# Kernel tuning notes

Hardware: AMD Instinct MI355X
Metric: run time of the kernel (lower is better)

The kernel has to match this reference:

```python
import jax, jax.numpy as jnp
import numpy as np
import math

SAMPLE_RATIO = 0.25
K = 5
EPS = 1e-6

def _cells(loc_orig, H, W):
    # map normalized [-1,1] coords to nearest grid cell index, as in tcformer token2map/map2token
    loc = jnp.clip(loc_orig, -1.0, 1.0)
    px = jnp.clip(jnp.round(0.5 * (loc[..., 0] + 1.0) * W - 0.5).astype(jnp.int32), 0, W - 1)
    py = jnp.clip(jnp.round(0.5 * (loc[..., 1] + 1.0) * H - 0.5).astype(jnp.int32), 0, H - 1)
    return py * W + px  # [B, N0]

def token2map(x, loc_orig, idx_agg, H, W):
    B, N, C = x.shape
    N0 = loc_orig.shape[1]
    cell = _cells(loc_orig, H, W)
    seg = (cell + jnp.arange(B)[:, None] * (H * W)).reshape(-1)
    feat = x[jnp.arange(B)[:, None], idx_agg]  # [B, N0, C] token feature per original point
    sums = jax.ops.segment_sum(feat.reshape(-1, C), seg, num_segments=B * H * W)
    cnt = jax.ops.segment_sum(jnp.ones((B * N0,), x.dtype), seg, num_segments=B * H * W)
    x_map = sums / (cnt[:, None] + EPS)  # per-cell mean over points hitting the cell
    return x_map.reshape(B, H, W, C).transpose(0, 3, 1, 2)

def map2token(x_map, N, loc_orig, idx_agg, agg_weight):
    B, C, H, W = x_map.shape
    cell = _cells(loc_orig, H, W)
    val = x_map.reshape(B, C, H * W).transpose(0, 2, 1)  # [B, HW, C]
    vpt = val[jnp.arange(B)[:, None], cell]              # [B, N0, C] map value at each point
    seg = (idx_agg + jnp.arange(B)[:, None] * N).reshape(-1)
    w = agg_weight.reshape(-1)
    wsum = jax.ops.segment_sum(w, seg, num_segments=B * N) + EPS
    ssum = jax.ops.segment_sum(vpt.reshape(-1, C) * w[:, None], seg, num_segments=B * N)
    return (ssum / wsum[:, None]).reshape(B, N, C)  # agg_weight-weighted mean per token

def token_cluster_merge(x, Ns, idx_agg, weight, k):
    B, N, C = x.shape
    # DPC-KNN clustering (index computation; mirrors torch.no_grad block)
    sq = jnp.sum(x * x, -1)
    d2 = jnp.clip(sq[:, :, None] + sq[:, None, :] - 2.0 * jnp.einsum('bnc,bmc->bnm', x, x), 0.0, None)
    dist = jnp.sqrt(d2) / (C ** 0.5)
    dnear = -jax.lax.top_k(-dist, k)[0]                  # k smallest distances (incl. self)
    density = jnp.exp(-jnp.mean(dnear * dnear, -1))
    mask = density[:, None, :] > density[:, :, None]
    dmax = jnp.max(dist.reshape(B, -1), -1)[:, None, None]
    parent_dist = jnp.min(jnp.where(mask, dist, dmax), -1)  # dist to nearest higher-density token
    score = parent_dist * density
    index_down = jax.lax.top_k(score, Ns)[1]             # [B, Ns] cluster centers
    idx_cluster = jnp.argmin(dist[jnp.arange(B)[:, None], index_down], axis=1)  # [B, N]
    idx_cluster = idx_cluster.at[jnp.arange(B)[:, None], index_down].set(jnp.arange(Ns)[None, :])
    # weighted merge of tokens into clusters
    seg = (idx_cluster + jnp.arange(B)[:, None] * Ns).reshape(-1)
    w = weight.reshape(-1)
    allw = jax.ops.segment_sum(w, seg, num_segments=B * Ns) + EPS
    norm_w = (w / allw[seg]).reshape(B, N)
    x_merged = jax.ops.segment_sum((x * norm_w[:, :, None]).reshape(-1, C), seg, num_segments=B * Ns).reshape(B, Ns, C)
    idx_agg_down = idx_cluster[jnp.arange(B)[:, None], idx_agg]      # compose index maps
    weight_t = norm_w[jnp.arange(B)[:, None], idx_agg][..., None]    # [B, N0, 1]
    return x_merged, idx_agg_down, weight_t

def _forward(x, loc_orig, idx_agg, agg_weight, idx_k_loc, H, W, conv_w, conv_b, skip_w, ln_g, ln_b, conf_w, conf_b):
    B, N, C = x.shape
    x_map = token2map(x, loc_orig, idx_agg, H, W)
    x_map = jax.lax.conv_general_dilated(x_map, conv_w, (2, 2), ((1, 1), (1, 1))) + conv_b[None, :, None, None]
    x_tok = map2token(x_map, N, loc_orig, idx_agg, agg_weight) + jnp.einsum('bnc,oc->bno', x, skip_w)
    mu = jnp.mean(x_tok, -1, keepdims=True)
    var = jnp.mean((x_tok - mu) ** 2, -1, keepdims=True)
    x_tok = (x_tok - mu) / jnp.sqrt(var + 1e-5) * ln_g + ln_b
    conf = jnp.einsum('bnc,oc->bno', x_tok, conf_w) + conf_b
    weight = jnp.exp(conf)
    Ns = max(math.ceil(N * SAMPLE_RATIO), 1)
    x_down, idx_agg_down, weight_t = token_cluster_merge(x_tok, Ns, idx_agg, weight, K)
    agg_weight_down = agg_weight * weight_t
    agg_weight_down = agg_weight_down / jnp.max(agg_weight_down, axis=1, keepdims=True)
    # down_block is an injected submodule; treated as identity passthrough here
    return x_down, idx_agg_down, agg_weight_down

def setup_inputs():
    key = jax.random.key(0)
    ks = jax.random.split(key, 8)
    B, N, C, N0, Cout = 8, 256, 256, 16384, 512
    return {
        'x': jax.random.normal(ks[0], (B, N, C), jnp.float32),
        'loc_orig': jax.random.uniform(ks[1], (B, N0, 2), jnp.float32, -1.0, 1.0),
        'idx_agg': jax.random.randint(ks[2], (B, N0), 0, N),
        'agg_weight': jax.random.uniform(ks[3], (B, N0, 1), jnp.float32, 0.1, 1.0),
        'idx_k_loc': jax.random.randint(ks[4], (B, N0, K), 0, N0),
        'H': 64, 'W': 64,
        'conv_w': jax.random.normal(ks[5], (Cout, C, 3, 3), jnp.float32) * 0.02,
        'conv_b': jnp.zeros((Cout,), jnp.float32),
        'skip_w': jax.random.normal(ks[6], (Cout, C), jnp.float32) * 0.02,
        'ln_g': jnp.ones((Cout,), jnp.float32),
        'ln_b': jnp.zeros((Cout,), jnp.float32),
        'conf_w': jax.random.normal(ks[7], (1, Cout), jnp.float32) * 0.02,
        'conf_b': jnp.zeros((1,), jnp.float32),
    }

def reference(x, loc_orig, idx_agg, agg_weight, idx_k_loc, H, W, conv_w, conv_b, skip_w, ln_g, ln_b, conf_w, conf_b):
    return _forward(x, loc_orig, idx_agg, agg_weight, idx_k_loc, H, W, conv_w, conv_b, skip_w, ln_g, ln_b, conf_w, conf_b)
```

## Files before the change

### kernel.cpp

```cpp
#include <hip/hip_runtime.h>
#include <math.h>

typedef unsigned long long ull;
typedef __attribute__((ext_vector_type(8))) short short8v;
typedef __attribute__((ext_vector_type(4))) float float4v;

#define NB   8
#define NTOK 256
#define CIN  256
#define NP   16384
#define NCO  512
#define HW64 4096
#define OHW  1024
#define NS   64
#define EPS  1e-6f
#define KC   2304

constexpr size_t OFF_SUMS = 0;
constexpr size_t OFF_CNT  = OFF_SUMS + (size_t)NB*HW64*CIN;
constexpr size_t OFF_AMAT = OFF_CNT  + (size_t)NB*HW64;
constexpr size_t OFF_ALLW = OFF_AMAT + (size_t)NB*NTOK*OHW;
constexpr size_t OFF_DMAX = OFF_ALLW + (size_t)NB*NS;
constexpr size_t OFF_MAXW = OFF_DMAX + NB;
constexpr size_t ZERO_END = OFF_MAXW + NB;
constexpr size_t OFF_WT   = ZERO_END;
constexpr size_t OFF_SKWT = OFF_WT   + (size_t)KC*NCO;
constexpr size_t OFF_Y    = OFF_SKWT + (size_t)CIN*NCO;
constexpr size_t OFF_C2   = OFF_Y    + (size_t)NB*OHW*NCO;
constexpr size_t OFF_WSUM = OFF_C2   + (size_t)NB*NTOK*NCO;
constexpr size_t OFF_XSKIP= OFF_WSUM + (size_t)NB*NTOK;
constexpr size_t OFF_XTOK = OFF_XSKIP+ (size_t)NB*NTOK*NCO;
constexpr size_t OFF_XPK  = OFF_XTOK + (size_t)NB*NTOK*NCO;
constexpr size_t OFF_WEXP = OFF_XPK  + (size_t)NB*NTOK*NCO;
constexpr size_t OFF_SQ   = OFF_WEXP + (size_t)NB*NTOK;
constexpr size_t OFF_DIST = OFF_SQ   + (size_t)NB*NTOK;
constexpr size_t OFF_DENS = OFF_DIST + (size_t)NB*NTOK*NTOK;
constexpr size_t OFF_SCORE= OFF_DENS + (size_t)NB*NTOK;
constexpr size_t OFF_IND  = OFF_SCORE+ (size_t)NB*NTOK;
constexpr size_t OFF_IDXCL= OFF_IND  + (size_t)NB*NS;
constexpr size_t OFF_NORMW= OFF_IDXCL+ (size_t)NB*NTOK;
constexpr size_t OFF_AWBUF= OFF_NORMW+ (size_t)NB*NTOK;
constexpr size_t OFF_XTPK = OFF_AWBUF+ (size_t)NB*NP;
constexpr size_t OFF_AMATP = OFF_SUMS;
constexpr size_t OFF_XTOKPK= OFF_Y;

__device__ __forceinline__ unsigned pack_hl(float x) {
    unsigned u = __float_as_uint(x);
    unsigned t = u + 0x7fffu + ((u >> 16) & 1u);
    unsigned hibits = t & 0xffff0000u;
    float lo = x - __uint_as_float(hibits);
    unsigned ul = __float_as_uint(lo);
    unsigned lt = ul + 0x7fffu + ((ul >> 16) & 1u);
    return hibits | (lt >> 16);
}
__device__ __forceinline__ unsigned hp2(unsigned w0, unsigned w1) {
    return __builtin_amdgcn_perm(w1, w0, 0x07060302u);
}
__device__ __forceinline__ unsigned lp2(unsigned w0, unsigned w1) {
    return __builtin_amdgcn_perm(w1, w0, 0x05040100u);
}

__global__ void hist(const float* __restrict__ loc, const int* __restrict__ idxagg,
                     const float* __restrict__ aggw,
                     int* __restrict__ cntmat, float* __restrict__ cnt,
                     float* __restrict__ amat) {
    int bp = blockIdx.x*256 + threadIdx.x;
    int b  = bp >> 14;
    float lx = loc[2*bp+0], ly = loc[2*bp+1];
    lx = fminf(fmaxf(lx, -1.f), 1.f);
    ly = fminf(fmaxf(ly, -1.f), 1.f);
    int px = (int)rintf((lx + 1.f)*32.f - 0.5f); px = min(max(px,0),63);
    int py = (int)rintf((ly + 1.f)*32.f - 0.5f); py = min(max(py,0),63);
    int cell = py*64 + px;
    int tok = idxagg[bp];
    atomicAdd(&cntmat[((size_t)(b*HW64 + cell))*NTOK + tok], 1);
    atomicAdd(&cnt[b*HW64 + cell], 1.0f);
    int qx = (int)rintf((lx + 1.f)*16.f - 0.5f); qx = min(max(qx,0),31);
    int qy = (int)rintf((ly + 1.f)*16.f - 0.5f); qy = min(max(qy,0),31);
    atomicAdd(&amat[((size_t)(b*NTOK + tok))*OHW + qy*32 + qx], aggw[bp]);
}

__global__ void cnt_pack(unsigned* __restrict__ m) {
    size_t i = (size_t)blockIdx.x*256 + threadIdx.x;
    int4 v = ((const int4*)m)[i];
    uint4 o;
    o.x = pack_hl((float)v.x); o.y = pack_hl((float)v.y);
    o.z = pack_hl((float)v.z); o.w = pack_hl((float)v.w);
    ((uint4*)m)[i] = o;
}

__global__ void xt_pack(const float* __restrict__ x, unsigned* __restrict__ xtpk) {
    int id = blockIdx.x*256 + threadIdx.x;
    int tok = id & 255, cin = (id >> 8) & 255, b = id >> 16;
    xtpk[id] = pack_hl(x[((size_t)(b*NTOK + tok))*CIN + cin]);
}

__global__ void wtrans(const float* __restrict__ convw, unsigned* __restrict__ wt) {
    int id = blockIdx.x*256 + threadIdx.x;
    int cout = id / KC, k = id - cout*KC;
    int grp = k >> 8, cin = k & 255;
    wt[id] = pack_hl(convw[(size_t)cout*KC + cin*9 + grp]);
}

__global__ void pack4(const float4* __restrict__ src, uint4* __restrict__ dst) {
    size_t i = (size_t)blockIdx.x*256 + threadIdx.x;
    float4 v = src[i];
    uint4 o;
    o.x = pack_hl(v.x); o.y = pack_hl(v.y); o.z = pack_hl(v.z); o.w = pack_hl(v.w);
    dst[i] = o;
}

__launch_bounds__(256)
__global__ void conv_gemm(const unsigned* __restrict__ xmap, const unsigned* __restrict__ wt,
                          const float* __restrict__ convb, unsigned* __restrict__ ytp) {
    __shared__ __align__(16) unsigned short Ahi[4096], Alo[4096];
    __shared__ __align__(16) unsigned short Bhi[2048], Blo[2048];
    int n0 = blockIdx.x * 128;
    int m0 = blockIdx.y * 64;
    int t = threadIdx.x;
    int lane = t & 63, wid = t >> 6;
    int wm = wid >> 1, wn = wid & 1;
    int l15 = lane & 15, l4 = lane >> 4;

    int rowL = t & 127, kg = t >> 7;
    int posG = n0 + rowL;
    int bb = posG >> 10, rem = posG & 1023;
    int oy = rem >> 5, ox = rem & 31;
    int rowB = t & 63, kgB = t >> 6;
    const unsigned* brow = wt + (size_t)(m0 + rowB)*KC + kgB*8;

    int wbA0 = (rowL>>4)*512 + kg*128 + (rowL&15)*8;
    int wbA1 = wbA0 + 256;
    int wbB  = (rowB>>4)*512 + kgB*128 + (rowB&15)*8;

    float4v acc[4][2] = {};
    uint4 a00,a01,a10,a11, b0,b1;

    auto loadA = [&](int kc) {
        int grp = kc >> 3;
        int ky = grp/3, kx = grp - 3*ky;
        int iy = 2*oy - 1 + ky, ix = 2*ox - 1 + kx;
        if ((unsigned)iy < 64u && (unsigned)ix < 64u) {
            const unsigned* ap = xmap + ((((size_t)bb*64 + iy)*64 + ix)*256 + (kc&7)*32 + kg*8);
            a00 = *(const uint4*)ap;       a01 = *(const uint4*)(ap + 4);
            a10 = *(const uint4*)(ap + 16); a11 = *(const uint4*)(ap + 20);
        } else {
            a00 = make_uint4(0,0,0,0); a01 = a00; a10 = a00; a11 = a00;
        }
    };
    auto loadB = [&](int kc) {
        const unsigned* bp = brow + (size_t)kc*32;
        b0 = *(const uint4*)bp; b1 = *(const uint4*)(bp + 4);
    };
    loadA(0); loadB(0);

    for (int kc = 0; kc < KC/32; ++kc) {
        __syncthreads();
        uint4 h, l;
        h.x=hp2(a00.x,a00.y); h.y=hp2(a00.z,a00.w); h.z=hp2(a01.x,a01.y); h.w=hp2(a01.z,a01.w);
        l.x=lp2(a00.x,a00.y); l.y=lp2(a00.z,a00.w); l.z=lp2(a01.x,a01.y); l.w=lp2(a01.z,a01.w);
        *(uint4*)&Ahi[wbA0] = h; *(uint4*)&Alo[wbA0] = l;
        h.x=hp2(a10.x,a10.y); h.y=hp2(a10.z,a10.w); h.z=hp2(a11.x,a11.y); h.w=hp2(a11.z,a11.w);
        l.x=lp2(a10.x,a10.y); l.y=lp2(a10.z,a10.w); l.z=lp2(a11.x,a11.y); l.w=lp2(a11.z,a11.w);
        *(uint4*)&Ahi[wbA1] = h; *(uint4*)&Alo[wbA1] = l;
        h.x=hp2(b0.x,b0.y); h.y=hp2(b0.z,b0.w); h.z=hp2(b1.x,b1.y); h.w=hp2(b1.z,b1.w);
        l.x=lp2(b0.x,b0.y); l.y=lp2(b0.z,b0.w); l.z=lp2(b1.x,b1.y); l.w=lp2(b1.z,b1.w);
        *(uint4*)&Bhi[wbB] = h; *(uint4*)&Blo[wbB] = l;
        __syncthreads();
        if (kc + 1 < KC/32) { loadA(kc+1); loadB(kc+1); }

        short8v bh[2], bl[2];
        #pragma unroll
        for (int q = 0; q < 2; ++q) {
            int off = (wn*2 + q)*512 + l4*128 + l15*8;
            bh[q] = *(const short8v*)&Bhi[off];
            bl[q] = *(const short8v*)&Blo[off];
        }
        #pragma unroll
        for (int p = 0; p < 4; ++p) {
            int off = (wm*4 + p)*512 + l4*128 + l15*8;
            short8v ah = *(const short8v*)&Ahi[off];
            short8v al = *(const short8v*)&Alo[off];
            #pragma unroll
            for (int q = 0; q < 2; ++q) {
                acc[p][q] = __builtin_amdgcn_mfma_f32_16x16x32_bf16(ah, bh[q], acc[p][q], 0, 0, 0);
                acc[p][q] = __builtin_amdgcn_mfma_f32_16x16x32_bf16(ah, bl[q], acc[p][q], 0, 0, 0);
                acc[p][q] = __builtin_amdgcn_mfma_f32_16x16x32_bf16(al, bh[q], acc[p][q], 0, 0, 0);
            }
        }
    }

    int bbk = n0 >> 10;
    int pos0 = (n0 & 1023) + wm*64;
    #pragma unroll
    for (int p = 0; p < 4; ++p) {
        int posb = pos0 + p*16 + l4*4;
        #pragma unroll
        for (int q = 0; q < 2; ++q) {
            int col = m0 + wn*32 + q*16 + l15;
            float bv = convb[col];
            uint4 o;
            o.x = pack_hl(acc[p][q][0] + bv);
            o.y = pack_hl(acc[p][q][1] + bv);
            o.z = pack_hl(acc[p][q][2] + bv);
            o.w = pack_hl(acc[p][q][3] + bv);
            *(uint4*)&ytp[((size_t)(bbk*NCO + col))*OHW + posb] = o;
        }
    }
}

template<int MODE, int TM, int TN>
__launch_bounds__(256)
__global__ void gemm_pk(const unsigned* __restrict__ A, const unsigned* __restrict__ B,
                        float* __restrict__ C, int K, int N,
                        long sA, long sB, long sC,
                        const float* __restrict__ aux, unsigned* __restrict__ dmaxU) {
    constexpr int NA = TM/64, NBs = TN/64;
    constexpr int WSM = TM/64;
    constexpr int WSN = 4/WSM;
    constexpr int TWM = TM/WSM, TWN = TN/WSN;
    constexpr int P = TWM/16, Q = TWN/16;
    __shared__ __align__(16) unsigned short Ahi[TM*32], Alo[TM*32];
    __shared__ __align__(16) unsigned short Bhi[TN*32], Blo[TN*32];
    int z = blockIdx.z;
    const unsigned* Ab = A + (size_t)z*sA;
    const unsigned* Bb = B + (size_t)z*sB;
    float* Cb = C + (size_t)z*sC;
    int n0 = blockIdx.x*TN, m0 = blockIdx.y*TM;
    int t = threadIdx.x;
    int lane = t & 63, wid = t >> 6;
    int wm = (WSM==2) ? (wid >> 1) : 0;
    int wn = (WSM==2) ? (wid & 1)  : wid;
    int l15 = lane & 15, l4 = lane >> 4;

    int rowA = t & (TM-1), kgA = t / TM;
    int rowB = t & (TN-1), kgB = t / TN;
    const unsigned* arow = Ab + (size_t)(m0 + rowA)*K + kgA*8;
    const unsigned* brw  = Bb + (size_t)(n0 + rowB)*K + kgB*8;
    int wbA = (rowA>>4)*512 + kgA*128 + (rowA&15)*8;
    int wbB = (rowB>>4)*512 + kgB*128 + (rowB&15)*8;

    float4v acc[P][Q] = {};
    uint4 ra[NA][2], rb[NBs][2];
    auto loadA = [&](int kc) {
        #pragma unroll
        for (int s = 0; s < NA; ++s) {
            const unsigned* p = arow + (size_t)kc*32 + s*16;
            ra[s][0] = *(const uint4*)p; ra[s][1] = *(const uint4*)(p + 4);
        }
    };
    auto loadB = [&](int kc) {
        #pragma unroll
        for (int s = 0; s < NBs; ++s) {
            const unsigned* p = brw + (size_t)kc*32 + s*16;
            rb[s][0] = *(const uint4*)p; rb[s][1] = *(const uint4*)(p + 4);
        }
    };
    loadA(0); loadB(0);
    int nkc = K >> 5;

    for (int kc = 0; kc < nkc; ++kc) {
        __syncthreads();
        uint4 h, l;
        #pragma unroll
        for (int s = 0; s < NA; ++s) {
            uint4 u0 = ra[s][0], u1 = ra[s][1];
            h.x=hp2(u0.x,u0.y); h.y=hp2(u0.z,u0.w); h.z=hp2(u1.x,u1.y); h.w=hp2(u1.z,u1.w);
            l.x=lp2(u0.x,u0.y); l.y=lp2(u0.z,u0.w); l.z=lp2(u1.x,u1.y); l.w=lp2(u1.z,u1.w);
            *(uint4*)&Ahi[wbA + s*256] = h; *(uint4*)&Alo[wbA + s*256] = l;
        }
        #pragma unroll
        for (int s = 0; s < NBs; ++s) {
            uint4 u0 = rb[s][0], u1 = rb[s][1];
            h.x=hp2(u0.x,u0.y); h.y=hp2(u0.z,u0.w); h.z=hp2(u1.x,u1.y); h.w=hp2(u1.z,u1.w);
            l.x=lp2(u0.x,u0.y); l.y=lp2(u0.z,u0.w); l.z=lp2(u1.x,u1.y); l.w=lp2(u1.z,u1.w);
            *(uint4*)&Bhi[wbB + s*256] = h; *(uint4*)&Blo[wbB + s*256] = l;
        }
        __syncthreads();
        if (kc + 1 < nkc) { loadA(kc+1); loadB(kc+1); }

        short8v bh[Q], bl[Q];
        #pragma unroll
        for (int q = 0; q < Q; ++q) {
            int off = (wn*Q + q)*512 + l4*128 + l15*8;
            bh[q] = *(const short8v*)&Bhi[off];
            bl[q] = *(const short8v*)&Blo[off];
        }
        #pragma unroll
        for (int p = 0; p < P; ++p) {
            int off = (wm*P + p)*512 + l4*128 + l15*8;
            short8v ah = *(const short8v*)&Ahi[off];
            short8v al = *(const short8v*)&Alo[off];
            #pragma unroll
            for (int q = 0; q < Q; ++q) {
                acc[p][q] = __builtin_amdgcn_mfma_f32_16x16x32_bf16(ah, bh[q], acc[p][q], 0, 0, 0);
                acc[p][q] = __builtin_amdgcn_mfma_f32_16x16x32_bf16(ah, bl[q], acc[p][q], 0, 0, 0);
                acc[p][q] = __builtin_amdgcn_mfma_f32_16x16x32_bf16(al, bh[q], acc[p][q], 0, 0, 0);
            }
        }
    }

    if (MODE == 0) {
        #pragma unroll
        for (int p = 0; p < P; ++p) {
            int mb = m0 + wm*TWM + p*16 + l4*4;
            #pragma unroll
            for (int q = 0; q < Q; ++q) {
                int n = n0 + wn*TWN + q*16 + l15;
                #pragma unroll
                for (int r = 0; r < 4; ++r)
                    Cb[(size_t)(mb + r)*N + n] = acc[p][q][r];
            }
        }
    } else if (MODE == 1) {
        const float inv = 1.0f / sqrtf(512.0f);
        const float* sqb = aux + (size_t)z*NTOK;
        float tmax = 0.f;
        #pragma unroll
        for (int p = 0; p < P; ++p) {
            int mb = m0 + wm*TWM + p*16 + l4*4;
            #pragma unroll
            for (int q = 0; q < Q; ++q) {
                int n = n0 + wn*TWN + q*16 + l15;
                float sn = sqb[n];
                #pragma unroll
                for (int r = 0; r < 4; ++r) {
                    float d2 = sqb[mb + r] + sn - 2.0f*acc[p][q][r];
                    float d = sqrtf(fmaxf(d2, 0.0f)) * inv;
                    Cb[(size_t)(mb + r)*N + n] = d;
                    tmax = fmaxf(tmax, d);
                }
            }
        }
        __shared__ float redm[4];
        #pragma unroll
        for (int off = 32; off; off >>= 1) tmax = fmaxf(tmax, __shfl_xor(tmax, off, 64));
        if (lane == 0) redm[wid] = tmax;
        __syncthreads();
        if (t == 0) {
            float m = fmaxf(fmaxf(redm[0], redm[1]), fmaxf(redm[2], redm[3]));
            atomicMax(dmaxU + z, __float_as_uint(m));
        }
    } else {
        unsigned* Cu = (unsigned*)Cb;
        const float* cntb = aux + (size_t)z*HW64;
        #pragma unroll
        for (int p = 0; p < P; ++p) {
            int mb = m0 + wm*TWM + p*16 + l4*4;
            #pragma unroll
            for (int q = 0; q < Q; ++q) {
                int n = n0 + wn*TWN + q*16 + l15;
                #pragma unroll
                for (int r = 0; r < 4; ++r) {
                    float v = acc[p][q][r] / (cntb[mb + r] + EPS);
                    Cu[(size_t)(mb + r)*N + n] = pack_hl(v);
                }
            }
        }
    }
}

__global__ void wsum_rows(const float* __restrict__ amat, float* __restrict__ wsum) {
    int row = blockIdx.x*4 + (threadIdx.x >> 6);
    int lane = threadIdx.x & 63;
    const float* ar = amat + (size_t)row*OHW;
    float s = 0.f;
    #pragma unroll
    for (int r = 0; r < 16; ++r) s += ar[lane + 64*r];
    #pragma unroll
    for (int off = 32; off; off >>= 1) s += __shfl_xor(s, off, 64);
    if (lane == 0) wsum[row] = s;
}

__device__ __forceinline__ float block_sum256(float v, float* red) {
    #pragma unroll
    for (int off = 32; off; off >>= 1) v += __shfl_xor(v, off, 64);
    __syncthreads();
    if ((threadIdx.x & 63) == 0) red[threadIdx.x >> 6] = v;
    __syncthreads();
    return red[0] + red[1] + red[2] + red[3];
}

__global__ void ln_conf(const float* __restrict__ C2, const float* __restrict__ wsum,
                        const float* __restrict__ xskip, const float* __restrict__ g,
                        const float* __restrict__ be, const float* __restrict__ confw,
                        const float* __restrict__ confb, float* __restrict__ xtok,
                        unsigned* __restrict__ xtokpk,
                        float* __restrict__ wexp, float* __restrict__ sqv) {
    __shared__ float red[4];
    int row = blockIdx.x, t = threadIdx.x;
    float ws = wsum[row] + EPS;
    size_t base = (size_t)row*NCO;
    float v0 = C2[base + t]       / ws + xskip[base + t];
    float v1 = C2[base + t + 256] / ws + xskip[base + t + 256];
    float mu  = block_sum256(v0 + v1, red) / 512.0f;
    float d0 = v0 - mu, d1 = v1 - mu;
    float var = block_sum256(d0*d0 + d1*d1, red) / 512.0f;
    float sv = sqrtf(var + 1e-5f);
    float x0 = d0/sv * g[t]       + be[t];
    float x1 = d1/sv * g[t + 256] + be[t + 256];
    xtok[base + t] = x0;
    xtok[base + t + 256] = x1;
    xtokpk[base + t] = pack_hl(x0);
    xtokpk[base + t + 256] = pack_hl(x1);
    float cs = block_sum256(x0*confw[t] + x1*confw[t + 256], red);
    float qs = block_sum256(x0*x0 + x1*x1, red);
    if (t == 0) {
        wexp[row] = expf(cs + confb[0]);
        sqv[row]  = qs;
    }
}

__global__ void knn_dens(const float* __restrict__ dist, float* __restrict__ dens) {
    int row = blockIdx.x*4 + (threadIdx.x >> 6);
    int lane = threadIdx.x & 63;
    const float* dr = dist + (size_t)row*NTOK;
    float v0 = dr[lane], v1 = dr[lane+64], v2 = dr[lane+128], v3 = dr[lane+192];
    float acc = 0.f;
    #pragma unroll
    for (int it = 0; it < 5; ++it) {
        float lm = fminf(fminf(v0, v1), fminf(v2, v3));
        float gm = lm;
        #pragma unroll
        for (int off = 32; off; off >>= 1) gm = fminf(gm, __shfl_xor(gm, off, 64));
        acc += gm*gm;
        ull ball = __ballot(lm == gm);
        int first = __ffsll(ball) - 1;
        if (lane == first) {
            if      (v0 == gm) v0 = 1e30f;
            else if (v1 == gm) v1 = 1e30f;
            else if (v2 == gm) v2 = 1e30f;
            else               v3 = 1e30f;
        }
    }
    if (lane == 0) dens[row] = expf(-(acc/5.0f));
}

__global__ void parent_score(const float* __restrict__ dist, const float* __restrict__ dens,
                             const unsigned* __restrict__ dmaxU, float* __restrict__ score) {
    int row = blockIdx.x*4 + (threadIdx.x >> 6);
    int lane = threadIdx.x & 63;
    int b = row >> 8;
    float di = dens[row];
    float dm = __uint_as_float(dmaxU[b]);
    const float* dr = dist + (size_t)row*NTOK;
    const float* db = dens + (size_t)b*NTOK;
    float pd = dm;
    #pragma unroll
    for (int r = 0; r < 4; ++r) {
        int j = lane + 64*r;
        pd = fminf(pd, (db[j] > di) ? dr[j] : dm);
    }
    #pragma unroll
    for (int off = 32; off; off >>= 1) pd = fminf(pd, __shfl_xor(pd, off, 64));
    if (lane == 0) score[row] = pd * di;
}

__global__ void topk64(const float* __restrict__ score, int* __restrict__ ind) {
    int b = blockIdx.x, lane = threadIdx.x;
    const float* sb = score + b*NTOK;
    ull k0, k1, k2, k3;
    {
        unsigned i0 = lane, i1 = lane+64, i2 = lane+128, i3 = lane+192;
        k0 = ((ull)(__float_as_uint(sb[i0]) + 1u) << 32) | (unsigned)(4095 - i0);
        k1 = ((ull)(__float_as_uint(sb[i1]) + 1u) << 32) | (unsigned)(4095 - i1);
        k2 = ((ull)(__float_as_uint(sb[i2]) + 1u) << 32) | (unsigned)(4095 - i2);
        k3 = ((ull)(__float_as_uint(sb[i3]) + 1u) << 32) | (unsigned)(4095 - i3);
    }
    for (int it = 0; it < 64; ++it) {
        ull lm = k0;
        if (k1 > lm) lm = k1;
        if (k2 > lm) lm = k2;
        if (k3 > lm) lm = k3;
        ull gm = lm;
        #pragma unroll
        for (int off = 32; off; off >>= 1) {
            ull o = __shfl_xor(gm, off, 64);
            if (o > gm) gm = o;
        }
        if (lane == 0) ind[b*NS + it] = 4095 - (int)(gm & 0xffffffffull);
        if      (k0 == gm) k0 = 0;
        else if (k1 == gm) k1 = 0;
        else if (k2 == gm) k2 = 0;
        else if (k3 == gm) k3 = 0;
    }
}

__global__ void assign_k(const float* __restrict__ dist, const int* __restrict__ ind,
                         int* __restrict__ idxcl) {
    int row = blockIdx.x*4 + (threadIdx.x >> 6);
    int lane = threadIdx.x & 63;
    int b = row >> 8, i = row & 255;
    int center = ind[b*NS + lane];
    float d = dist[((size_t)(b*NTOK + center))*NTOK + i];
    ull key = ((ull)__float_as_uint(d) << 32) | (unsigned)lane;
    #pragma unroll
    for (int off = 32; off; off >>= 1) {
        ull o = __shfl_xor(key, off, 64);
        if (o < key) key = o;
    }
    if (lane == 0) idxcl[row] = (int)(key & 0xffffffffull);
}

__global__ void center_set(const int* __restrict__ ind, int* __restrict__ idxcl) {
    int id = threadIdx.x;
    int b = id >> 6, s = id & 63;
    idxcl[b*NTOK + ind[id]] = s;
}

__global__ void allw_acc(const int* __restrict__ idxcl, const float* __restrict__ wexp,
                         float* __restrict__ allw) {
    int b = blockIdx.x, i = threadIdx.x;
    atomicAdd(&allw[b*NS + idxcl[b*NTOK + i]], wexp[b*NTOK + i]);
}

__global__ void normw_k(const int* __restrict__ idxcl, const float* __restrict__ wexp,
                        const float* __restrict__ allw, float* __restrict__ normw) {
    int b = blockIdx.x, i = threadIdx.x;
    normw[b*NTOK + i] = wexp[b*NTOK + i] / (allw[b*NS + idxcl[b*NTOK + i]] + EPS);
}

__global__ void merge_k(const float* __restrict__ xtok, const int* __restrict__ idxcl,
                        const float* __restrict__ normw, float* __restrict__ xout) {
    int row = blockIdx.x, t = threadIdx.x;
    int b = row >> 8;
    int cl = idxcl[row];
    float nw = normw[row];
    float* o = xout + ((size_t)(b*NS + cl))*NCO;
    const float* xr = xtok + (size_t)row*NCO;
    atomicAdd(&o[t],       xr[t]       * nw);
    atomicAdd(&o[t + 256], xr[t + 256] * nw);
}

__global__ void out_idx_aw(const int* __restrict__ idxagg, const float* __restrict__ aggw,
                           const int* __restrict__ idxcl, const float* __restrict__ normw,
                           float* __restrict__ dout, float* __restrict__ awbuf,
                           unsigned* __restrict__ maxw) {
    __shared__ float red[4];
    int bp = blockIdx.x*256 + threadIdx.x;
    int b = bp >> 14;
    int tok = idxagg[bp];
    int cl = idxcl[b*NTOK + tok];
    dout[(size_t)NB*NS*NCO + bp] = (float)cl;
    float aw = aggw[bp] * normw[b*NTOK + tok];
    awbuf[bp] = aw;
    float m = aw;
    #pragma unroll
    for (int off = 32; off; off >>= 1) m = fmaxf(m, __shfl_xor(m, off, 64));
    if ((threadIdx.x & 63) == 0) red[threadIdx.x >> 6] = m;
    __syncthreads();
    if (threadIdx.x == 0) {
        float mm = fmaxf(fmaxf(red[0], red[1]), fmaxf(red[2], red[3]));
        atomicMax(&maxw[b], __float_as_uint(mm));
    }
}

__global__ void aw_final(const float* __restrict__ awbuf, const float* __restrict__ maxw,
                         float* __restrict__ dout) {
    int bp = blockIdx.x*256 + threadIdx.x;
    int b = bp >> 14;
    dout[(size_t)NB*NS*NCO + (size_t)NB*NP + bp] = awbuf[bp] / maxw[b];
}

extern "C" void kernel_launch(void* const* d_in, const int* in_sizes, int n_in,
                              void* d_out, int out_size, void* d_ws, size_t ws_size,
                              hipStream_t stream) {
    const float* x      = (const float*)d_in[0];
    const float* loc    = (const float*)d_in[1];
    const int*   idxagg = (const int*)  d_in[2];
    const float* aggw   = (const float*)d_in[3];
    const float* convw  = (const float*)d_in[7];
    const float* convb  = (const float*)d_in[8];
    const float* skipw  = (const float*)d_in[9];
    const float* lng    = (const float*)d_in[10];
    const float* lnb    = (const float*)d_in[11];
    const float* confw  = (const float*)d_in[12];
    const float* confb  = (const float*)d_in[13];

    float* ws = (float*)d_ws;
    float* dout = (float*)d_out;

    (void)hipMemsetAsync(ws, 0, ZERO_END*sizeof(float), stream);
    (void)hipMemsetAsync(dout, 0, (size_t)NB*NS*NCO*sizeof(float), stream);

    hist<<<dim3(NB*NP/256), 256, 0, stream>>>(loc, idxagg, aggw,
                                              (int*)(ws + OFF_SUMS), ws + OFF_CNT, ws + OFF_AMAT);
    cnt_pack<<<dim3(NB*HW64*CIN/1024), 256, 0, stream>>>((unsigned*)(ws + OFF_SUMS));
    xt_pack<<<dim3(NB*CIN*NTOK/256), 256, 0, stream>>>(x, (unsigned*)(ws + OFF_XTPK));
    wtrans<<<dim3(KC*NCO/256), 256, 0, stream>>>(convw, (unsigned*)(ws + OFF_WT));
    pack4<<<dim3(CIN*NCO/1024), 256, 0, stream>>>((const float4*)skipw, (uint4*)(ws + OFF_SKWT));
    pack4<<<dim3(NB*NTOK*CIN/1024), 256, 0, stream>>>((const float4*)x, (uint4*)(ws + OFF_XPK));

    gemm_pk<2,128,128><<<dim3(2, 32, 8), 256, 0, stream>>>((const unsigned*)(ws + OFF_SUMS),
                                                   (const unsigned*)(ws + OFF_XTPK),
                                                   ws + OFF_SUMS, NTOK, CIN,
                                                   (long)HW64*NTOK, (long)CIN*NTOK, (long)HW64*CIN,
                                                   ws + OFF_CNT, nullptr);

    conv_gemm<<<dim3(64, 8), 256, 0, stream>>>((const unsigned*)(ws + OFF_SUMS),
                                               (const unsigned*)(ws + OFF_WT), convb,
                                               (unsigned*)(ws + OFF_Y));

    wsum_rows<<<dim3(NB*NTOK/4), 256, 0, stream>>>(ws + OFF_AMAT, ws + OFF_WSUM);
    pack4<<<dim3(NB*NTOK*OHW/1024), 256, 0, stream>>>((const float4*)(ws + OFF_AMAT),
                                                      (uint4*)(ws + OFF_AMATP));
    gemm_pk<0,64,64><<<dim3(8, 4, 8), 256, 0, stream>>>((const unsigned*)(ws + OFF_AMATP),
                                                  (const unsigned*)(ws + OFF_Y),
                                                  ws + OFF_C2, OHW, NCO,
                                                  (long)NTOK*OHW, (long)NCO*OHW, (long)NTOK*NCO,
                                                  nullptr, nullptr);
    gemm_pk<0,64,64><<<dim3(8, 32, 1), 256, 0, stream>>>((const unsigned*)(ws + OFF_XPK),
                                                   (const unsigned*)(ws + OFF_SKWT),
                                                   ws + OFF_XSKIP, CIN, NCO, 0, 0, 0,
                                                   nullptr, nullptr);

    ln_conf<<<dim3(NB*NTOK), 256, 0, stream>>>(ws + OFF_C2, ws + OFF_WSUM, ws + OFF_XSKIP,
                                               lng, lnb, confw, confb,
                                               ws + OFF_XTOK, (unsigned*)(ws + OFF_XTOKPK),
                                               ws + OFF_WEXP, ws + OFF_SQ);

    gemm_pk<1,64,64><<<dim3(4, 4, 8), 256, 0, stream>>>((const unsigned*)(ws + OFF_XTOKPK),
                                                  (const unsigned*)(ws + OFF_XTOKPK),
                                                  ws + OFF_DIST, NCO, NTOK,
                                                  (long)NTOK*NCO, (long)NTOK*NCO, (long)NTOK*NTOK,
                                                  ws + OFF_SQ, (unsigned*)(ws + OFF_DMAX));

    knn_dens<<<dim3(NB*NTOK/4), 256, 0, stream>>>(ws + OFF_DIST, ws + OFF_DENS);
    parent_score<<<dim3(NB*NTOK/4), 256, 0, stream>>>(ws + OFF_DIST, ws + OFF_DENS,
                                                      (const unsigned*)(ws + OFF_DMAX), ws + OFF_SCORE);
    topk64<<<dim3(NB), 64, 0, stream>>>(ws + OFF_SCORE, (int*)(ws + OFF_IND));
    assign_k<<<dim3(NB*NTOK/4), 256, 0, stream>>>(ws + OFF_DIST, (const int*)(ws + OFF_IND),
                                                  (int*)(ws + OFF_IDXCL));
    center_set<<<dim3(1), 512, 0, stream>>>((const int*)(ws + OFF_IND), (int*)(ws + OFF_IDXCL));
    allw_acc<<<dim3(NB), 256, 0, stream>>>((const int*)(ws + OFF_IDXCL), ws + OFF_WEXP, ws + OFF_ALLW);
    normw_k<<<dim3(NB), 256, 0, stream>>>((const int*)(ws + OFF_IDXCL), ws + OFF_WEXP,
                                          ws + OFF_ALLW, ws + OFF_NORMW);
    merge_k<<<dim3(NB*NTOK), 256, 0, stream>>>(ws + OFF_XTOK, (const int*)(ws + OFF_IDXCL),
                                               ws + OFF_NORMW, dout);
    out_idx_aw<<<dim3(NB*NP/256), 256, 0, stream>>>(idxagg, aggw, (const int*)(ws + OFF_IDXCL),
                                                    ws + OFF_NORMW, dout, ws + OFF_AWBUF,
                                                    (unsigned*)(ws + OFF_MAXW));
    aw_final<<<dim3(NB*NP/256), 256, 0, stream>>>(ws + OFF_AWBUF, (const float*)(ws + OFF_MAXW), dout);
}
```

Measured before the change: 321.1 us.

## Pre-split conv weights into MFMA fragment layout and double-buffer A tiles

The weight transform now writes conv weights already split into hi/lo bf16 halves and arranged in per-lane MFMA fragment order, so conv_gemm loads B fragments straight from global memory into registers without staging them through LDS. The A tile uses two LDS buffers, so the next tile's load and repack overlap the current MFMAs and each iteration needs one barrier instead of two. This removes B's LDS traffic and hi/lo conversion from the hot loop, at the cost of more registers for prefetched B fragments and double the A LDS footprint.

```diff
diff --git a/kernel.cpp b/kernel.cpp
--- a/kernel.cpp
+++ b/kernel.cpp
@@ -15,6 +15,7 @@
 #define NS   64
 #define EPS  1e-6f
 #define KC   2304
+#define NKC  72
 
 constexpr size_t OFF_SUMS = 0;
 constexpr size_t OFF_CNT  = OFF_SUMS + (size_t)NB*HW64*CIN;
@@ -95,11 +96,29 @@
     xtpk[id] = pack_hl(x[((size_t)(b*NTOK + tok))*CIN + cin]);
 }
 
-__global__ void wtrans(const float* __restrict__ convw, unsigned* __restrict__ wt) {
-    int id = blockIdx.x*256 + threadIdx.x;
-    int cout = id / KC, k = id - cout*KC;
-    int grp = k >> 8, cin = k & 255;
-    wt[id] = pack_hl(convw[(size_t)cout*KC + cin*9 + grp]);
+__global__ void wtrans(const float* __restrict__ convw, uint4* __restrict__ wtf) {
+    int tid = blockIdx.x*256 + threadIdx.x;
+    int lane = tid & 63;
+    int r1 = tid >> 6;
+    int h = r1 & 1;
+    int r2 = r1 >> 1;
+    int f = r2 & 3;
+    int r3 = r2 >> 2;
+    int kc = r3 % NKC, mt = r3 / NKC;
+    int cout = mt*64 + f*16 + (lane & 15);
+    int kb = kc*32 + (lane >> 4)*8;
+    unsigned s[8];
+    #pragma unroll
+    for (int j = 0; j < 8; ++j) {
+        int k = kb + j;
+        int grp = k >> 8, cin = k & 255;
+        unsigned w = pack_hl(convw[(size_t)cout*KC + cin*9 + grp]);
+        s[j] = h ? (w & 0xffffu) : (w >> 16);
+    }
+    uint4 o;
+    o.x = s[0] | (s[1]<<16); o.y = s[2] | (s[3]<<16);
+    o.z = s[4] | (s[5]<<16); o.w = s[6] | (s[7]<<16);
+    wtf[tid] = o;
 }
 
 __global__ void pack4(const float4* __restrict__ src, uint4* __restrict__ dst) {
@@ -111,12 +130,12 @@
 }
 
 __launch_bounds__(256)
-__global__ void conv_gemm(const unsigned* __restrict__ xmap, const unsigned* __restrict__ wt,
+__global__ void conv_gemm(const unsigned* __restrict__ xmap, const uint4* __restrict__ wtf,
                           const float* __restrict__ convb, unsigned* __restrict__ ytp) {
-    __shared__ __align__(16) unsigned short Ahi[4096], Alo[4096];
-    __shared__ __align__(16) unsigned short Bhi[2048], Blo[2048];
+    __shared__ __align__(16) unsigned short Ahi[2][4096], Alo[2][4096];
     int n0 = blockIdx.x * 128;
-    int m0 = blockIdx.y * 64;
+    int mt = blockIdx.y;
+    int m0 = mt * 64;
     int t = threadIdx.x;
     int lane = t & 63, wid = t >> 6;
     int wm = wid >> 1, wn = wid & 1;
@@ -126,15 +145,12 @@
     int posG = n0 + rowL;
     int bb = posG >> 10, rem = posG & 1023;
     int oy = rem >> 5, ox = rem & 31;
-    int rowB = t & 63, kgB = t >> 6;
-    const unsigned* brow = wt + (size_t)(m0 + rowB)*KC + kgB*8;
 
     int wbA0 = (rowL>>4)*512 + kg*128 + (rowL&15)*8;
     int wbA1 = wbA0 + 256;
-    int wbB  = (rowB>>4)*512 + kgB*128 + (rowB&15)*8;
 
     float4v acc[4][2] = {};
-    uint4 a00,a01,a10,a11, b0,b1;
+    uint4 a00,a01,a10,a11;
 
     auto loadA = [&](int kc) {
         int grp = kc >> 3;
@@ -148,46 +164,58 @@
             a00 = make_uint4(0,0,0,0); a01 = a00; a10 = a00; a11 = a00;
         }
     };
-    auto loadB = [&](int kc) {
-        const unsigned* bp = brow + (size_t)kc*32;
-        b0 = *(const uint4*)bp; b1 = *(const uint4*)(bp + 4);
-    };
-    loadA(0); loadB(0);
-
-    for (int kc = 0; kc < KC/32; ++kc) {
-        __syncthreads();
+    auto repackA = [&](int buf) {
         uint4 h, l;
         h.x=hp2(a00.x,a00.y); h.y=hp2(a00.z,a00.w); h.z=hp2(a01.x,a01.y); h.w=hp2(a01.z,a01.w);
         l.x=lp2(a00.x,a00.y); l.y=lp2(a00.z,a00.w); l.z=lp2(a01.x,a01.y); l.w=lp2(a01.z,a01.w);
-        *(uint4*)&Ahi[wbA0] = h; *(uint4*)&Alo[wbA0] = l;
+        *(uint4*)&Ahi[buf][wbA0] = h; *(uint4*)&Alo[buf][wbA0] = l;
         h.x=hp2(a10.x,a10.y); h.y=hp2(a10.z,a10.w); h.z=hp2(a11.x,a11.y); h.w=hp2(a11.z,a11.w);
         l.x=lp2(a10.x,a10.y); l.y=lp2(a10.z,a10.w); l.z=lp2(a11.x,a11.y); l.w=lp2(a11.z,a11.w);
-        *(uint4*)&Ahi[wbA1] = h; *(uint4*)&Alo[wbA1] = l;
-        h.x=hp2(b0.x,b0.y); h.y=hp2(b0.z,b0.w); h.z=hp2(b1.x,b1.y); h.w=hp2(b1.z,b1.w);
-        l.x=lp2(b0.x,b0.y); l.y=lp2(b0.z,b0.w); l.z=lp2(b1.x,b1.y); l.w=lp2(b1.z,b1.w);
-        *(uint4*)&Bhi[wbB] = h; *(uint4*)&Blo[wbB] = l;
-        __syncthreads();
-        if (kc + 1 < KC/32) { loadA(kc+1); loadB(kc+1); }
-
-        short8v bh[2], bl[2];
-        #pragma unroll
-        for (int q = 0; q < 2; ++q) {
-            int off = (wn*2 + q)*512 + l4*128 + l15*8;
-            bh[q] = *(const short8v*)&Bhi[off];
-            bl[q] = *(const short8v*)&Blo[off];
+        *(uint4*)&Ahi[buf][wbA1] = h; *(uint4*)&Alo[buf][wbA1] = l;
+    };
+    const uint4* wbase = wtf + ((size_t)(((mt*NKC)*4 + wn*2)*2))*64 + lane;
+
+    short8v bhc[2], blc[2], bhn[2], bln[2];
+    #pragma unroll
+    for (int q = 0; q < 2; ++q) {
+        bhc[q] = *(const short8v*)(wbase + q*128);
+        blc[q] = *(const short8v*)(wbase + q*128 + 64);
+    }
+    loadA(0);
+    repackA(0);
+    __syncthreads();
+    int cur = 0;
+
+    for (int kc = 0; kc < NKC; ++kc) {
+        bool notlast = (kc + 1 < NKC);
+        if (notlast) {
+            loadA(kc+1);
+            const uint4* wb = wbase + (size_t)(kc+1)*512;
+            #pragma unroll
+            for (int q = 0; q < 2; ++q) {
+                bhn[q] = *(const short8v*)(wb + q*128);
+                bln[q] = *(const short8v*)(wb + q*128 + 64);
+            }
         }
         #pragma unroll
         for (int p = 0; p < 4; ++p) {
             int off = (wm*4 + p)*512 + l4*128 + l15*8;
-            short8v ah = *(const short8v*)&Ahi[off];
-            short8v al = *(const short8v*)&Alo[off];
+            short8v ah = *(const short8v*)&Ahi[cur][off];
+            short8v al = *(const short8v*)&Alo[cur][off];
             #pragma unroll
             for (int q = 0; q < 2; ++q) {
-                acc[p][q] = __builtin_amdgcn_mfma_f32_16x16x32_bf16(ah, bh[q], acc[p][q], 0, 0, 0);
-                acc[p][q] = __builtin_amdgcn_mfma_f32_16x16x32_bf16(ah, bl[q], acc[p][q], 0, 0, 0);
-                acc[p][q] = __builtin_amdgcn_mfma_f32_16x16x32_bf16(al, bh[q], acc[p][q], 0, 0, 0);
+                acc[p][q] = __builtin_amdgcn_mfma_f32_16x16x32_bf16(ah, bhc[q], acc[p][q], 0, 0, 0);
+                acc[p][q] = __builtin_amdgcn_mfma_f32_16x16x32_bf16(ah, blc[q], acc[p][q], 0, 0, 0);
+                acc[p][q] = __builtin_amdgcn_mfma_f32_16x16x32_bf16(al, bhc[q], acc[p][q], 0, 0, 0);
             }
         }
+        if (notlast) {
+            repackA(cur ^ 1);
+            #pragma unroll
+            for (int q = 0; q < 2; ++q) { bhc[q] = bhn[q]; blc[q] = bln[q]; }
+        }
+        __syncthreads();
+        cur ^= 1;
     }
 
     int bbk = n0 >> 10;
@@ -587,7 +615,7 @@
                                               (int*)(ws + OFF_SUMS), ws + OFF_CNT, ws + OFF_AMAT);
     cnt_pack<<<dim3(NB*HW64*CIN/1024), 256, 0, stream>>>((unsigned*)(ws + OFF_SUMS));
     xt_pack<<<dim3(NB*CIN*NTOK/256), 256, 0, stream>>>(x, (unsigned*)(ws + OFF_XTPK));
-    wtrans<<<dim3(KC*NCO/256), 256, 0, stream>>>(convw, (unsigned*)(ws + OFF_WT));
+    wtrans<<<dim3(1152), 256, 0, stream>>>(convw, (uint4*)(ws + OFF_WT));
     pack4<<<dim3(CIN*NCO/1024), 256, 0, stream>>>((const float4*)skipw, (uint4*)(ws + OFF_SKWT));
     pack4<<<dim3(NB*NTOK*CIN/1024), 256, 0, stream>>>((const float4*)x, (uint4*)(ws + OFF_XPK));
 
@@ -598,7 +626,7 @@
                                                    ws + OFF_CNT, nullptr);
 
     conv_gemm<<<dim3(64, 8), 256, 0, stream>>>((const unsigned*)(ws + OFF_SUMS),
-                                               (const unsigned*)(ws + OFF_WT), convb,
+                                               (const uint4*)(ws + OFF_WT), convb,
                                                (unsigned*)(ws + OFF_Y));
 
     wsum_rows<<<dim3(NB*NTOK/4), 256, 0, stream>>>(ws + OFF_AMAT, ws + OFF_WSUM);
```

Result: faster. 304.3 us (-5.2%).
